# Kernel optimization log

Measured on AMD Instinct MI355X. Metric: run time of the kernel, lower is better.

Reference implementation:

```python
import jax, jax.numpy as jnp
import numpy as np

D = 896      # mm_hidden_size
H = 8        # num heads
HD = D // H  # head dim = 112
M = 8        # num_memory_tokens
P = 196      # patch_size
EPS = 1e-12


def _layernorm(x, g, b):
    mu = jnp.mean(x, axis=-1, keepdims=True)
    var = jnp.mean(jnp.square(x - mu), axis=-1, keepdims=True)
    return (x - mu) * jax.lax.rsqrt(var + EPS) * g + b


def setup_inputs() -> dict:
    key = jax.random.key(0)
    ks = jax.random.split(key, 12)
    F = 32
    s = 0.02
    return {
        "image_features": jax.random.normal(ks[0], (F, P, D), jnp.float32),
        "initial_memory": jax.random.normal(ks[1], (M, P, D), jnp.float32),
        "qW": jax.random.normal(ks[2], (D, D), jnp.float32) * s,
        "qb": jnp.zeros((D,), jnp.float32),
        "kW": jax.random.normal(ks[3], (D, D), jnp.float32) * s,
        "kb": jnp.zeros((D,), jnp.float32),
        "vW": jax.random.normal(ks[4], (D, D), jnp.float32) * s,
        "vb": jnp.zeros((D,), jnp.float32),
        "oW": jax.random.normal(ks[5], (D, D), jnp.float32) * s,
        "ob": jnp.zeros((D,), jnp.float32),
        "ln1_g": jnp.ones((D,), jnp.float32),
        "ln1_b": jnp.zeros((D,), jnp.float32),
        "mW": jax.random.normal(ks[6], (D, 4 * D), jnp.float32) * s,
        "mb": jnp.zeros((4 * D,), jnp.float32),
        "pW": jax.random.normal(ks[7], (4 * D, D), jnp.float32) * s,
        "pb": jnp.zeros((D,), jnp.float32),
        "ln2_g": jnp.ones((D,), jnp.float32),
        "ln2_b": jnp.zeros((D,), jnp.float32),
    }


def reference(image_features, initial_memory, qW, qb, kW, kb, vW, vb,
              oW, ob, ln1_g, ln1_b, mW, mb, pW, pb, ln2_g, ln2_b):
    F = image_features.shape[0]
    Lq = M * P            # 1568 query tokens
    Lk = F * P            # kv tokens
    mem = initial_memory.reshape(1, Lq, D)      # [1, Lq, D]
    img = image_features.reshape(1, Lk, D)      # [1, Lk, D]

    def heads(x, L):
        return x.reshape(1, L, H, HD).transpose(0, 2, 1, 3)  # [1,H,L,hd]

    q = heads(mem @ qW + qb, Lq)
    k = heads(img @ kW + kb, Lk)
    v = heads(img @ vW + vb, Lk)

    scores = jnp.einsum('bhqd,bhkd->bhqk', q, k) / np.sqrt(HD).astype(jnp.float32)
    probs = jax.nn.softmax(scores, axis=-1)                  # [1,H,Lq,Lk]
    ctx = jnp.einsum('bhqk,bhkd->bhqd', probs, v)
    ctx = ctx.transpose(0, 2, 1, 3).reshape(1, Lq, D)

    # residual + layernorm epilogue of Attention
    attn_out = _layernorm(ctx @ oW + ob + mem, ln1_g, ln1_b)

    # MLP -> residual + layernorm
    hidden = jax.nn.relu(attn_out @ mW + mb)                 # [1, Lq, 4D]
    out = _layernorm(hidden @ pW + pb + attn_out, ln2_g, ln2_b)

    # frame attention scores: sum over heads and query tokens, avg per frame
    attn_sum = probs.sum(axis=(1, 2))[0]                     # [Lk]
    frame_scores = attn_sum.reshape(F, P).mean(axis=1)       # [F]

    final_memory = out.reshape(M, P, D)
    return final_memory, frame_scores
```

## Files before the change

kernel.cpp:

```cpp
#include <hip/hip_runtime.h>
#include <hip/hip_bf16.h>
#include <math.h>

#define TP_D   896
#define TP_H   8
#define TP_HD  112
#define TP_LQ  1568
#define TP_LK  6272
#define TP_D4  3584
#define TP_F   32
#define TP_P   196

typedef unsigned short u16;
typedef float f32x4 __attribute__((ext_vector_type(4)));
typedef __bf16 bf16x8 __attribute__((ext_vector_type(8)));

__device__ inline float bf2f(u16 u) {
    return __uint_as_float(((unsigned int)u) << 16);
}
__device__ inline u16 f2bf(float f) {
    unsigned int x = __float_as_uint(f);
    unsigned int lsb = (x >> 16) & 1u;
    x += 0x7fffu + lsb;
    return (u16)(x >> 16);
}
__device__ inline ushort4 pack4(float a, float b, float c, float d) {
    return make_ushort4(f2bf(a), f2bf(b), f2bf(c), f2bf(d));
}
__device__ inline int pidx(int row, int col) {
    return row * 128 + (col ^ ((row & 7) << 3));
}
__device__ inline void gl_lds16(const u16* g, u16* l) {
    __builtin_amdgcn_global_load_lds(
        (const __attribute__((address_space(1))) unsigned int*)g,
        (__attribute__((address_space(3))) unsigned int*)l,
        16, 0, 0);
}

__global__ void cast2_f32_bf16(const float* __restrict__ src0, u16* __restrict__ dst0, int n0,
                               const float* __restrict__ src1, u16* __restrict__ dst1, int n1) {
    int i = (blockIdx.x * blockDim.x + threadIdx.x) * 4;
    const float* s; u16* d; int n;
    if (i < n0) { s = src0; d = dst0; n = n0; }
    else        { i -= n0; s = src1; d = dst1; n = n1; if (i >= n) return; }
    float4 v = *(const float4*)(s + i);
    *(ushort4*)(d + i) = pack4(v.x, v.y, v.z, v.w);
}

__global__ void cast_div_bf16(const float* __restrict__ src, const float* __restrict__ l,
                              u16* __restrict__ dst) {
    int i = (blockIdx.x * 256 + threadIdx.x) * 4;
    if (i >= TP_LQ * TP_D) return;
    int q = i / TP_D;
    int col = i - q * TP_D;
    int h = col / TP_HD;
    float inv = 1.f / l[h * TP_LQ + q];
    float4 v = *(const float4*)(src + i);
    *(ushort4*)(dst + i) = pack4(v.x * inv, v.y * inv, v.z * inv, v.w * inv);
}

__global__ void transpose_cast(const float* __restrict__ src, u16* __restrict__ dst, int R, int C) {
    __shared__ float t[32][33];
    int bx = blockIdx.x * 32;
    int by = blockIdx.y * 32;
    int tx = threadIdx.x, ty = threadIdx.y;
#pragma unroll
    for (int j = 0; j < 4; ++j)
        t[ty + j * 8][tx] = src[(size_t)(by + ty + j * 8) * C + bx + tx];
    __syncthreads();
#pragma unroll
    for (int j = 0; j < 4; ++j)
        dst[(size_t)(bx + ty + j * 8) * R + by + tx] = f2bf(t[tx][ty + j * 8]);
}

__global__ void transpose_cast4(const float* __restrict__ s0, u16* __restrict__ d0,
                                const float* __restrict__ s1, u16* __restrict__ d1,
                                const float* __restrict__ s2, u16* __restrict__ d2,
                                const float* __restrict__ s3, u16* __restrict__ d3) {
    __shared__ float t[32][33];
    const float* src; u16* dst;
    switch (blockIdx.z) {
        case 0: src = s0; dst = d0; break;
        case 1: src = s1; dst = d1; break;
        case 2: src = s2; dst = d2; break;
        default: src = s3; dst = d3; break;
    }
    int bx = blockIdx.x * 32;
    int by = blockIdx.y * 32;
    int tx = threadIdx.x, ty = threadIdx.y;
#pragma unroll
    for (int j = 0; j < 4; ++j)
        t[ty + j * 8][tx] = src[(size_t)(by + ty + j * 8) * TP_D + bx + tx];
    __syncthreads();
#pragma unroll
    for (int j = 0; j < 4; ++j)
        dst[(size_t)(bx + ty + j * 8) * TP_D + by + tx] = f2bf(t[tx][ty + j * 8]);
}

struct GemmParams {
    const u16* A;  int lda;
    const u16* Bt; int ldb;
    int M, N, K;
    const float* bias;
    float* outF;
    u16* outB; int ldc;
    int relu;
    int kc;
};

template <int MODE>
__global__ __launch_bounds__(256, 4) void gemm_bf16(GemmParams p) {
    __shared__ u16 lsA[128 * 32];
    __shared__ u16 lsB[64 * 32];

    const int tid = threadIdx.x;
    const int z = blockIdx.z;
    const u16* A  = p.A;
    const u16* Bt = p.Bt;
    if (MODE == 6) {
        A  += (size_t)z * p.kc;
        Bt += (size_t)z * p.kc;
    }
    const int m0 = blockIdx.y * 128;
    const int n0 = blockIdx.x * 64;

    const int lane = tid & 63;
    const int w = tid >> 6;
    const int wm = (w >> 1) * 64, wn = (w & 1) * 32;
    const int c = lane & 15, q = lane >> 4;
    const int xq = (q ^ (c & 3)) << 3;

    f32x4 acc[4][2];
#pragma unroll
    for (int i = 0; i < 4; ++i) { acc[i][0] = 0.f; acc[i][1] = 0.f; }

    const int lrow = lane >> 2;
    const int lchunk = (lane & 3) ^ (lrow & 3);
    int ga_row0 = m0 + w * 32 + lrow;      if (ga_row0 >= p.M) ga_row0 = p.M - 1;
    int ga_row1 = m0 + w * 32 + 16 + lrow; if (ga_row1 >= p.M) ga_row1 = p.M - 1;
    int gb_row  = n0 + w * 16 + lrow;      if (gb_row  >= p.N) gb_row  = p.N - 1;
    const u16* gA0 = A  + (size_t)ga_row0 * p.lda + lchunk * 8;
    const u16* gA1 = A  + (size_t)ga_row1 * p.lda + lchunk * 8;
    const u16* gB  = Bt + (size_t)gb_row  * p.ldb + lchunk * 8;
    u16* lA0 = &lsA[(w * 32) * 32];
    u16* lA1 = &lsA[(w * 32 + 16) * 32];
    u16* lB  = &lsB[(w * 16) * 32];

    const int KT = p.K >> 5;
    for (int kt = 0; kt < KT; ++kt) {
        const int k0 = kt << 5;
        gl_lds16(gA0 + k0, lA0);
        gl_lds16(gA1 + k0, lA1);
        gl_lds16(gB + k0, lB);
        __syncthreads();

        bf16x8 af[4], bfv[2];
#pragma unroll
        for (int mi = 0; mi < 4; ++mi) {
            const int r = wm + mi * 16 + c;
            af[mi] = *(const bf16x8*)(&lsA[r * 32 + xq]);
        }
#pragma unroll
        for (int ni = 0; ni < 2; ++ni) {
            const int rb = wn + ni * 16 + c;
            bfv[ni] = *(const bf16x8*)(&lsB[rb * 32 + xq]);
        }
#pragma unroll
        for (int mi = 0; mi < 4; ++mi)
#pragma unroll
            for (int ni = 0; ni < 2; ++ni)
                acc[mi][ni] = __builtin_amdgcn_mfma_f32_16x16x32_bf16(af[mi], bfv[ni], acc[mi][ni], 0, 0, 0);
        __syncthreads();
    }

#pragma unroll
    for (int mi = 0; mi < 4; ++mi) {
#pragma unroll
        for (int r = 0; r < 4; ++r) {
            const int row = m0 + wm + mi * 16 + q * 4 + r;
            if (row >= p.M) continue;
#pragma unroll
            for (int ni = 0; ni < 2; ++ni) {
                const int col = n0 + wn + ni * 16 + c;
                float v = acc[mi][ni][r];
                if (MODE == 4) {
                    v += p.bias[col];
                    if (p.relu) v = v > 0.f ? v : 0.f;
                    p.outB[(size_t)row * p.ldc + col] = f2bf(v);
                } else if (MODE == 6) {
                    atomicAdd(&p.outF[(size_t)row * p.ldc + col], v);
                }
            }
        }
    }
}

__global__ __launch_bounds__(256, 4) void qkv_proj(
        const u16* __restrict__ imgB, const u16* __restrict__ memB,
        const u16* __restrict__ kWt, const u16* __restrict__ vWt, const u16* __restrict__ qWt,
        const float* __restrict__ kb, const float* __restrict__ vb, const float* __restrict__ qb,
        u16* __restrict__ Kf, u16* __restrict__ Vtf, u16* __restrict__ Qf) {
    __shared__ u16 lsA[128 * 32];
    __shared__ u16 lsB[64 * 32];

    const int z = blockIdx.z;
    const u16* A; const u16* Bt; const float* bias; int M;
    if (z == 0)      { A = imgB; Bt = kWt; bias = kb; M = TP_LK; }
    else if (z == 1) { A = imgB; Bt = vWt; bias = vb; M = TP_LK; }
    else             { A = memB; Bt = qWt; bias = qb; M = TP_LQ; }

    const int m0 = blockIdx.y * 128;
    if (m0 >= M) return;
    const int n0 = blockIdx.x * 64;

    const int tid = threadIdx.x;
    const int lane = tid & 63;
    const int w = tid >> 6;
    const int wm = (w >> 1) * 64, wn = (w & 1) * 32;
    const int c = lane & 15, q = lane >> 4;
    const int xq = (q ^ (c & 3)) << 3;

    f32x4 acc[4][2];
#pragma unroll
    for (int i = 0; i < 4; ++i) { acc[i][0] = 0.f; acc[i][1] = 0.f; }

    const int lrow = lane >> 2;
    const int lchunk = (lane & 3) ^ (lrow & 3);
    int ga_row0 = m0 + w * 32 + lrow;      if (ga_row0 >= M) ga_row0 = M - 1;
    int ga_row1 = m0 + w * 32 + 16 + lrow; if (ga_row1 >= M) ga_row1 = M - 1;
    const int gb_row = n0 + w * 16 + lrow;
    const u16* gA0 = A  + (size_t)ga_row0 * TP_D + lchunk * 8;
    const u16* gA1 = A  + (size_t)ga_row1 * TP_D + lchunk * 8;
    const u16* gB  = Bt + (size_t)gb_row  * TP_D + lchunk * 8;
    u16* lA0 = &lsA[(w * 32) * 32];
    u16* lA1 = &lsA[(w * 32 + 16) * 32];
    u16* lB  = &lsB[(w * 16) * 32];

    for (int kt = 0; kt < 28; ++kt) {
        const int k0 = kt << 5;
        gl_lds16(gA0 + k0, lA0);
        gl_lds16(gA1 + k0, lA1);
        gl_lds16(gB + k0, lB);
        __syncthreads();

        bf16x8 af[4], bfv[2];
#pragma unroll
        for (int mi = 0; mi < 4; ++mi) {
            const int r = wm + mi * 16 + c;
            af[mi] = *(const bf16x8*)(&lsA[r * 32 + xq]);
        }
#pragma unroll
        for (int ni = 0; ni < 2; ++ni) {
            const int rb = wn + ni * 16 + c;
            bfv[ni] = *(const bf16x8*)(&lsB[rb * 32 + xq]);
        }
#pragma unroll
        for (int mi = 0; mi < 4; ++mi)
#pragma unroll
            for (int ni = 0; ni < 2; ++ni)
                acc[mi][ni] = __builtin_amdgcn_mfma_f32_16x16x32_bf16(af[mi], bfv[ni], acc[mi][ni], 0, 0, 0);
        __syncthreads();
    }

    if (z == 1) {
#pragma unroll
        for (int ni = 0; ni < 2; ++ni) {
            const int col = n0 + wn + ni * 16 + c;
            const float bv = bias[col];
#pragma unroll
            for (int mi = 0; mi < 4; ++mi) {
                const int mbase = m0 + wm + mi * 16 + q * 4;
                f32x4 a = acc[mi][ni];
                *(ushort4*)(Vtf + (size_t)col * TP_LK + mbase) =
                    pack4(a[0] + bv, a[1] + bv, a[2] + bv, a[3] + bv);
            }
        }
        return;
    }

    u16* outB = (z == 0) ? Kf : Qf;
#pragma unroll
    for (int mi = 0; mi < 4; ++mi) {
#pragma unroll
        for (int r = 0; r < 4; ++r) {
            const int row = m0 + wm + mi * 16 + q * 4 + r;
            if (row >= M) continue;
#pragma unroll
            for (int ni = 0; ni < 2; ++ni) {
                const int col = n0 + wn + ni * 16 + c;
                outB[(size_t)row * TP_D + col] = f2bf(acc[mi][ni][r] + bias[col]);
            }
        }
    }
}

__global__ __launch_bounds__(256, 2) void attn_fused(
        const u16* __restrict__ Qf, const u16* __restrict__ Kf,
        const u16* __restrict__ Vtf, u16* __restrict__ E,
        float* __restrict__ lsum, float* __restrict__ ctxF, float scale) {
    __shared__ u16 lsQ[128 * 128];
    __shared__ u16 lsB[128 * 40];
    __shared__ u16 lsP[128 * 128];

    const int ks  = blockIdx.x;
    const int m0  = blockIdx.y * 128;
    const int h   = blockIdx.z;
    const int tid = threadIdx.x;
    const int lane = tid & 63, w = tid >> 6;
    const int wm = (w >> 1) * 64, wn = (w & 1) * 64;
    const int c = lane & 15, q = lane >> 4;

    {
        const int row = tid >> 1;
        const int half = (tid & 1) * 64;
        int qrow = m0 + row; if (qrow > TP_LQ - 1) qrow = TP_LQ - 1;
        const u16* src = Qf + (size_t)qrow * TP_D + h * TP_HD;
#pragma unroll
        for (int j = 0; j < 8; ++j) {
            int col = half + j * 8;
            uint4 v = make_uint4(0, 0, 0, 0);
            if (col + 8 <= TP_HD) v = *(const uint4*)(src + col);
            *(uint4*)(&lsQ[pidx(row, col)]) = v;
        }
    }

    const int r0 = tid >> 2;
    const int c8 = (tid & 3) * 8;
    const int keybase = ks * 896;

    f32x4 acc_pv[4][4];
#pragma unroll
    for (int i = 0; i < 4; ++i)
#pragma unroll
        for (int j = 0; j < 4; ++j) acc_pv[i][j] = 0.f;
    float rs[4] = {0.f, 0.f, 0.f, 0.f};

    for (int kb = 0; kb < 7; ++kb) {
        const int kblk = keybase + kb * 128;
        f32x4 acc_s[4][4];
#pragma unroll
        for (int i = 0; i < 4; ++i)
#pragma unroll
            for (int j = 0; j < 4; ++j) acc_s[i][j] = 0.f;

#pragma unroll
        for (int kt = 0; kt < 4; ++kt) {
            const int k0 = kt * 32;
            const bool valid = (k0 + c8 + 8) <= TP_HD;
            uint4 zv = make_uint4(0, 0, 0, 0);
            uint4 vb0 = valid ? *(const uint4*)(Kf + (size_t)(kblk + r0) * TP_D + h * TP_HD + k0 + c8) : zv;
            uint4 vb1 = valid ? *(const uint4*)(Kf + (size_t)(kblk + r0 + 64) * TP_D + h * TP_HD + k0 + c8) : zv;
            __syncthreads();
            *(uint4*)(&lsB[r0 * 40 + c8])        = vb0;
            *(uint4*)(&lsB[(r0 + 64) * 40 + c8]) = vb1;
            __syncthreads();
            bf16x8 af[4], bfv[4];
#pragma unroll
            for (int mi = 0; mi < 4; ++mi)
                af[mi] = *(const bf16x8*)(&lsQ[pidx(wm + mi * 16 + c, k0 + q * 8)]);
#pragma unroll
            for (int ni = 0; ni < 4; ++ni)
                bfv[ni] = *(const bf16x8*)(&lsB[(wn + ni * 16 + c) * 40 + q * 8]);
#pragma unroll
            for (int mi = 0; mi < 4; ++mi)
#pragma unroll
                for (int ni = 0; ni < 4; ++ni)
                    acc_s[mi][ni] = __builtin_amdgcn_mfma_f32_16x16x32_bf16(bfv[ni], af[mi], acc_s[mi][ni], 0, 0, 0);
        }

        __syncthreads();
#pragma unroll
        for (int mi = 0; mi < 4; ++mi) {
            const int prow = wm + mi * 16 + c;
            const int qr = m0 + prow;
            const bool qv = qr < TP_LQ;
            float rp = 0.f;
#pragma unroll
            for (int ni = 0; ni < 4; ++ni) {
                float e0, e1, e2, e3;
                {
                    f32x4 a = acc_s[mi][ni];
                    e0 = __expf(fminf(a[0] * scale, 30.f));
                    e1 = __expf(fminf(a[1] * scale, 30.f));
                    e2 = __expf(fminf(a[2] * scale, 30.f));
                    e3 = __expf(fminf(a[3] * scale, 30.f));
                }
                rp += (e0 + e1) + (e2 + e3);
                ushort4 pk = pack4(e0, e1, e2, e3);
                const int kcol = wn + ni * 16 + q * 4;
                if (qv)
                    *(ushort4*)(E + ((size_t)h * TP_LQ + qr) * TP_LK + kblk + kcol) = pk;
                *(ushort4*)(&lsP[pidx(prow, kcol)]) = pk;
            }
            rs[mi] += rp;
        }

#pragma unroll
        for (int kt = 0; kt < 4; ++kt) {
            const int kk = kblk + kt * 32 + c8;
            int d0 = r0;
            int d1 = r0 + 64; if (d1 > TP_HD - 1) d1 = TP_HD - 1;
            uint4 vb0 = *(const uint4*)(Vtf + ((size_t)h * TP_HD + d0) * TP_LK + kk);
            uint4 vb1 = *(const uint4*)(Vtf + ((size_t)h * TP_HD + d1) * TP_LK + kk);
            __syncthreads();
            *(uint4*)(&lsB[r0 * 40 + c8])        = vb0;
            *(uint4*)(&lsB[(r0 + 64) * 40 + c8]) = vb1;
            __syncthreads();
            bf16x8 ap[4], bv[4];
#pragma unroll
            for (int mi = 0; mi < 4; ++mi)
                ap[mi] = *(const bf16x8*)(&lsP[pidx(wm + mi * 16 + c, kt * 32 + q * 8)]);
#pragma unroll
            for (int ni = 0; ni < 4; ++ni)
                bv[ni] = *(const bf16x8*)(&lsB[(wn + ni * 16 + c) * 40 + q * 8]);
#pragma unroll
            for (int mi = 0; mi < 4; ++mi)
#pragma unroll
                for (int ni = 0; ni < 4; ++ni)
                    acc_pv[mi][ni] = __builtin_amdgcn_mfma_f32_16x16x32_bf16(ap[mi], bv[ni], acc_pv[mi][ni], 0, 0, 0);
        }
    }

#pragma unroll
    for (int mi = 0; mi < 4; ++mi) {
        float rp = rs[mi];
        rp += __shfl_xor(rp, 16, 64);
        rp += __shfl_xor(rp, 32, 64);
        const int qr = m0 + wm + mi * 16 + c;
        if (q == 0 && qr < TP_LQ) atomicAdd(&lsum[h * TP_LQ + qr], rp);
    }
#pragma unroll
    for (int mi = 0; mi < 4; ++mi) {
#pragma unroll
        for (int r = 0; r < 4; ++r) {
            const int qr = m0 + wm + mi * 16 + q * 4 + r;
            if (qr >= TP_LQ) continue;
#pragma unroll
            for (int ni = 0; ni < 4; ++ni) {
                const int d = wn + ni * 16 + c;
                if (d < TP_HD)
                    atomicAdd(&ctxF[(size_t)qr * TP_D + h * TP_HD + d], acc_pv[mi][ni][r]);
            }
        }
    }
}

__global__ void colsum_kernel(const u16* __restrict__ E, const float* __restrict__ l,
                              float* __restrict__ colsum, int nrows) {
    int c4 = blockIdx.x * 256 + threadIdx.x;
    if (c4 >= TP_LK / 4) return;
    int chunk = (nrows + gridDim.y - 1) / gridDim.y;
    int r0 = blockIdx.y * chunk;
    int r1 = r0 + chunk; if (r1 > nrows) r1 = nrows;
    float a0 = 0.f, a1 = 0.f, a2 = 0.f, a3 = 0.f;
    for (int r = r0; r < r1; ++r) {
        float inv = 1.f / l[r];
        ushort4 u = ((const ushort4*)(E + (size_t)r * TP_LK))[c4];
        a0 += bf2f(u.x) * inv; a1 += bf2f(u.y) * inv;
        a2 += bf2f(u.z) * inv; a3 += bf2f(u.w) * inv;
    }
    atomicAdd(&colsum[4 * c4 + 0], a0);
    atomicAdd(&colsum[4 * c4 + 1], a1);
    atomicAdd(&colsum[4 * c4 + 2], a2);
    atomicAdd(&colsum[4 * c4 + 3], a3);
}

__global__ __launch_bounds__(256) void layernorm_rows(const float* __restrict__ x,
        const float* __restrict__ bias, const float* __restrict__ res,
        const float* __restrict__ g, const float* __restrict__ b,
        float* __restrict__ outF, u16* __restrict__ outB) {
    const int tid = threadIdx.x;
    const float* xr = x + (size_t)blockIdx.x * TP_D;
    const float* rr = res + (size_t)blockIdx.x * TP_D;
    float v[4];
#pragma unroll
    for (int i = 0; i < 4; ++i) {
        int idx = tid + i * 256;
        v[i] = (idx < TP_D) ? (xr[idx] + bias[idx] + rr[idx]) : 0.f;
    }
    float s = v[0] + v[1] + v[2] + v[3];
    __shared__ float red[4];
#pragma unroll
    for (int o = 32; o > 0; o >>= 1) s += __shfl_xor(s, o, 64);
    if ((tid & 63) == 0) red[tid >> 6] = s;
    __syncthreads();
    const float mu = (red[0] + red[1] + red[2] + red[3]) * (1.f / TP_D);
    __syncthreads();
    float ss = 0.f;
#pragma unroll
    for (int i = 0; i < 4; ++i) {
        int idx = tid + i * 256;
        if (idx < TP_D) { float d = v[i] - mu; ss += d * d; }
    }
#pragma unroll
    for (int o = 32; o > 0; o >>= 1) ss += __shfl_xor(ss, o, 64);
    if ((tid & 63) == 0) red[tid >> 6] = ss;
    __syncthreads();
    const float var = (red[0] + red[1] + red[2] + red[3]) * (1.f / TP_D);
    const float rsq = rsqrtf(var + 1e-12f);
    float* of = outF + (size_t)blockIdx.x * TP_D;
    u16* obp = outB ? outB + (size_t)blockIdx.x * TP_D : nullptr;
#pragma unroll
    for (int i = 0; i < 4; ++i) {
        int idx = tid + i * 256;
        if (idx < TP_D) {
            float y = (v[i] - mu) * rsq * g[idx] + b[idx];
            of[idx] = y;
            if (obp) obp[idx] = f2bf(y);
        }
    }
}

__global__ void frame_scores_kernel(const float* __restrict__ colsum, float* __restrict__ out) {
    const int tid = threadIdx.x;
    float v = (tid < TP_P) ? colsum[blockIdx.x * TP_P + tid] : 0.f;
    __shared__ float red[4];
#pragma unroll
    for (int o = 32; o > 0; o >>= 1) v += __shfl_xor(v, o, 64);
    if ((tid & 63) == 0) red[tid >> 6] = v;
    __syncthreads();
    if (tid == 0) out[blockIdx.x] = (red[0] + red[1] + red[2] + red[3]) * (1.f / TP_P);
}

extern "C" void kernel_launch(void* const* d_in, const int* in_sizes, int n_in,
                              void* d_out, int out_size, void* d_ws, size_t ws_size,
                              hipStream_t stream) {
    const float* img  = (const float*)d_in[0];
    const float* mem  = (const float*)d_in[1];
    const float* qW   = (const float*)d_in[2];
    const float* qb   = (const float*)d_in[3];
    const float* kW   = (const float*)d_in[4];
    const float* kb   = (const float*)d_in[5];
    const float* vW   = (const float*)d_in[6];
    const float* vb   = (const float*)d_in[7];
    const float* oW   = (const float*)d_in[8];
    const float* ob   = (const float*)d_in[9];
    const float* ln1g = (const float*)d_in[10];
    const float* ln1b = (const float*)d_in[11];
    const float* mW   = (const float*)d_in[12];
    const float* mb   = (const float*)d_in[13];
    const float* pW   = (const float*)d_in[14];
    const float* pb   = (const float*)d_in[15];
    const float* ln2g = (const float*)d_in[16];
    const float* ln2b = (const float*)d_in[17];
    float* out = (float*)d_out;

    char* base = (char*)d_ws;
    size_t off = 0;
    auto take = [&](size_t nbytes) -> void* {
        void* p = base + off;
        off += (nbytes + 255) & ~(size_t)255;
        return p;
    };

    u16* imgB  = (u16*)take((size_t)TP_LK * TP_D * 2);
    u16* memB  = (u16*)take((size_t)TP_LQ * TP_D * 2);
    u16* qWt   = (u16*)take((size_t)TP_D * TP_D * 2);
    u16* kWt   = (u16*)take((size_t)TP_D * TP_D * 2);
    u16* vWt   = (u16*)take((size_t)TP_D * TP_D * 2);
    u16* oWt   = (u16*)take((size_t)TP_D * TP_D * 2);
    u16* mWt   = (u16*)take((size_t)TP_D * TP_D4 * 2);
    u16* pWt   = (u16*)take((size_t)TP_D * TP_D4 * 2);
    u16* Qf    = (u16*)take((size_t)TP_LQ * TP_D * 2);
    u16* Kf    = (u16*)take((size_t)TP_LK * TP_D * 2);
    u16* Vtf   = (u16*)take((size_t)TP_LK * TP_D * 2);
    u16* ctxB  = (u16*)take((size_t)TP_LQ * TP_D * 2);
    float* attn  = (float*)take((size_t)TP_LQ * TP_D * 4);
    u16* attnB = (u16*)take((size_t)TP_LQ * TP_D * 2);
    u16* hidden= (u16*)take((size_t)TP_LQ * TP_D4 * 2);
    u16* E     = (u16*)take((size_t)TP_H * TP_LQ * TP_LK * 2);
    float* ctxF  = (float*)take((size_t)TP_LQ * TP_D * 4);
    float* pre1  = (float*)take((size_t)TP_LQ * TP_D * 4);
    float* pre2  = (float*)take((size_t)TP_LQ * TP_D * 4);
    float* colsum= (float*)take((size_t)TP_LK * 4);
    float* lsum  = (float*)take((size_t)TP_H * TP_LQ * 4);
    size_t zlen = (char*)(lsum + TP_H * TP_LQ) - (char*)ctxF;

    {
        int n0 = TP_LK * TP_D, n1 = TP_LQ * TP_D;
        cast2_f32_bf16<<<((n0 + n1) / 4 + 255) / 256, 256, 0, stream>>>(img, imgB, n0, mem, memB, n1);
    }
    transpose_cast4<<<dim3(28, 28, 4), dim3(32, 8), 0, stream>>>(qW, qWt, kW, kWt, vW, vWt, oW, oWt);
    transpose_cast<<<dim3(TP_D4 / 32, TP_D / 32), dim3(32, 8), 0, stream>>>(mW, mWt, TP_D, TP_D4);
    transpose_cast<<<dim3(TP_D / 32, TP_D4 / 32), dim3(32, 8), 0, stream>>>(pW, pWt, TP_D4, TP_D);
    hipMemsetAsync(ctxF, 0, zlen, stream);

    qkv_proj<<<dim3(14, 49, 3), 256, 0, stream>>>(imgB, memB, kWt, vWt, qWt,
                                                  kb, vb, qb, Kf, Vtf, Qf);

    const float scale = 0.09449111825230679f;
    attn_fused<<<dim3(7, 13, TP_H), 256, 0, stream>>>(Qf, Kf, Vtf, E, lsum, ctxF, scale);
    colsum_kernel<<<dim3(7, 448), 256, 0, stream>>>(E, lsum, colsum, TP_H * TP_LQ);
    cast_div_bf16<<<(TP_LQ * TP_D / 4 + 255) / 256, 256, 0, stream>>>(ctxF, lsum, ctxB);

    {
        GemmParams p{};
        p.A = ctxB; p.lda = TP_D;
        p.Bt = oWt; p.ldb = TP_D;
        p.M = TP_LQ; p.N = TP_D; p.K = 448; p.kc = 448;
        p.outF = pre1; p.ldc = TP_D;
        gemm_bf16<6><<<dim3(14, 13, 2), 256, 0, stream>>>(p);
    }
    layernorm_rows<<<TP_LQ, 256, 0, stream>>>(pre1, ob, mem, ln1g, ln1b, attn, attnB);

    {
        GemmParams p{};
        p.A = attnB; p.lda = TP_D;
        p.Bt = mWt; p.ldb = TP_D;
        p.M = TP_LQ; p.N = TP_D4; p.K = TP_D;
        p.bias = mb; p.outB = hidden; p.ldc = TP_D4; p.relu = 1;
        gemm_bf16<4><<<dim3(56, 13, 1), 256, 0, stream>>>(p);
    }
    {
        GemmParams p{};
        p.A = hidden; p.lda = TP_D4;
        p.Bt = pWt; p.ldb = TP_D4;
        p.M = TP_LQ; p.N = TP_D; p.K = 896; p.kc = 896;
        p.outF = pre2; p.ldc = TP_D;
        gemm_bf16<6><<<dim3(14, 13, 4), 256, 0, stream>>>(p);
    }
    layernorm_rows<<<TP_LQ, 256, 0, stream>>>(pre2, pb, attn, ln2g, ln2b, out, nullptr);

    frame_scores_kernel<<<TP_F, 256, 0, stream>>>(colsum, out + (size_t)TP_LQ * TP_D);
}
```

Baseline: 498.5 us.

## Replace materialized exp matrix with per-row per-frame partial sums

The attention kernel no longer writes the full bf16 exponent matrix (8x1568x6272) to global memory. Instead it accumulates, for each query row and head, partial sums split into the one or two frames that each 128-key block spans, and writes them into a small [H*Lq, 32] buffer with atomics. A new finalize kernel derives the row sums from these partials, normalises them and reduces to frame scores. This removes the large global write and the column-sum re-read, at the cost of extra select and shuffle work plus more atomics inside the attention kernel.

```diff
diff --git a/kernel.cpp b/kernel.cpp
--- a/kernel.cpp
+++ b/kernel.cpp
@@ -296,8 +296,8 @@
 
 __global__ __launch_bounds__(256, 2) void attn_fused(
         const u16* __restrict__ Qf, const u16* __restrict__ Kf,
-        const u16* __restrict__ Vtf, u16* __restrict__ E,
-        float* __restrict__ lsum, float* __restrict__ ctxF, float scale) {
+        const u16* __restrict__ Vtf, float* __restrict__ FQ,
+        float* __restrict__ ctxF, float scale) {
     __shared__ u16 lsQ[128 * 128];
     __shared__ u16 lsB[128 * 40];
     __shared__ u16 lsP[128 * 128];
@@ -333,7 +333,6 @@
     for (int i = 0; i < 4; ++i)
 #pragma unroll
         for (int j = 0; j < 4; ++j) acc_pv[i][j] = 0.f;
-    float rs[4] = {0.f, 0.f, 0.f, 0.f};
 
     for (int kb = 0; kb < 7; ++kb) {
         const int kblk = keybase + kb * 128;
@@ -369,30 +368,35 @@
         }
 
         __syncthreads();
+        const int fA = kblk / TP_P;
+        const int bpos = (fA + 1) * TP_P - kblk;
+        const int kq = wn + q * 4;
 #pragma unroll
         for (int mi = 0; mi < 4; ++mi) {
             const int prow = wm + mi * 16 + c;
+            float accA = 0.f, accB = 0.f;
+#pragma unroll
+            for (int ni = 0; ni < 4; ++ni) {
+                f32x4 a = acc_s[mi][ni];
+                float e0 = __expf(fminf(a[0] * scale, 30.f));
+                float e1 = __expf(fminf(a[1] * scale, 30.f));
+                float e2 = __expf(fminf(a[2] * scale, 30.f));
+                float e3 = __expf(fminf(a[3] * scale, 30.f));
+                const int kl = kq + ni * 16;
+                accA += (kl + 0 < bpos) ? e0 : 0.f;  accB += (kl + 0 < bpos) ? 0.f : e0;
+                accA += (kl + 1 < bpos) ? e1 : 0.f;  accB += (kl + 1 < bpos) ? 0.f : e1;
+                accA += (kl + 2 < bpos) ? e2 : 0.f;  accB += (kl + 2 < bpos) ? 0.f : e2;
+                accA += (kl + 3 < bpos) ? e3 : 0.f;  accB += (kl + 3 < bpos) ? 0.f : e3;
+                *(ushort4*)(&lsP[pidx(prow, kl)]) = pack4(e0, e1, e2, e3);
+            }
+            accA += __shfl_xor(accA, 16, 64); accA += __shfl_xor(accA, 32, 64);
+            accB += __shfl_xor(accB, 16, 64); accB += __shfl_xor(accB, 32, 64);
             const int qr = m0 + prow;
-            const bool qv = qr < TP_LQ;
-            float rp = 0.f;
-#pragma unroll
-            for (int ni = 0; ni < 4; ++ni) {
-                float e0, e1, e2, e3;
-                {
-                    f32x4 a = acc_s[mi][ni];
-                    e0 = __expf(fminf(a[0] * scale, 30.f));
-                    e1 = __expf(fminf(a[1] * scale, 30.f));
-                    e2 = __expf(fminf(a[2] * scale, 30.f));
-                    e3 = __expf(fminf(a[3] * scale, 30.f));
-                }
-                rp += (e0 + e1) + (e2 + e3);
-                ushort4 pk = pack4(e0, e1, e2, e3);
-                const int kcol = wn + ni * 16 + q * 4;
-                if (qv)
-                    *(ushort4*)(E + ((size_t)h * TP_LQ + qr) * TP_LK + kblk + kcol) = pk;
-                *(ushort4*)(&lsP[pidx(prow, kcol)]) = pk;
+            if (q == 0 && qr < TP_LQ) {
+                float* fq = &FQ[((size_t)h * TP_LQ + qr) * TP_F];
+                atomicAdd(fq + fA, accA);
+                if (bpos < 128) atomicAdd(fq + fA + 1, accB);
             }
-            rs[mi] += rp;
         }
 
 #pragma unroll
@@ -423,14 +427,6 @@
 
 #pragma unroll
     for (int mi = 0; mi < 4; ++mi) {
-        float rp = rs[mi];
-        rp += __shfl_xor(rp, 16, 64);
-        rp += __shfl_xor(rp, 32, 64);
-        const int qr = m0 + wm + mi * 16 + c;
-        if (q == 0 && qr < TP_LQ) atomicAdd(&lsum[h * TP_LQ + qr], rp);
-    }
-#pragma unroll
-    for (int mi = 0; mi < 4; ++mi) {
 #pragma unroll
         for (int r = 0; r < 4; ++r) {
             const int qr = m0 + wm + mi * 16 + q * 4 + r;
@@ -445,24 +441,32 @@
     }
 }
 
-__global__ void colsum_kernel(const u16* __restrict__ E, const float* __restrict__ l,
-                              float* __restrict__ colsum, int nrows) {
-    int c4 = blockIdx.x * 256 + threadIdx.x;
-    if (c4 >= TP_LK / 4) return;
-    int chunk = (nrows + gridDim.y - 1) / gridDim.y;
-    int r0 = blockIdx.y * chunk;
-    int r1 = r0 + chunk; if (r1 > nrows) r1 = nrows;
-    float a0 = 0.f, a1 = 0.f, a2 = 0.f, a3 = 0.f;
-    for (int r = r0; r < r1; ++r) {
-        float inv = 1.f / l[r];
-        ushort4 u = ((const ushort4*)(E + (size_t)r * TP_LK))[c4];
-        a0 += bf2f(u.x) * inv; a1 += bf2f(u.y) * inv;
-        a2 += bf2f(u.z) * inv; a3 += bf2f(u.w) * inv;
-    }
-    atomicAdd(&colsum[4 * c4 + 0], a0);
-    atomicAdd(&colsum[4 * c4 + 1], a1);
-    atomicAdd(&colsum[4 * c4 + 2], a2);
-    atomicAdd(&colsum[4 * c4 + 3], a3);
+__global__ __launch_bounds__(256) void frame_finalize(
+        const float* __restrict__ FQ, float* __restrict__ lsum,
+        float* __restrict__ frame_out) {
+    __shared__ float red[256 * 33];
+    const int tid = threadIdx.x;
+    const int row = blockIdx.x * 256 + tid;
+    float v[32];
+    const float4* src = (const float4*)(FQ + (size_t)row * TP_F);
+    float l = 0.f;
+#pragma unroll
+    for (int i = 0; i < 8; ++i) {
+        float4 t = src[i];
+        v[4 * i + 0] = t.x; v[4 * i + 1] = t.y;
+        v[4 * i + 2] = t.z; v[4 * i + 3] = t.w;
+        l += (t.x + t.y) + (t.z + t.w);
+    }
+    lsum[row] = l;
+    const float inv = 1.f / l;
+#pragma unroll
+    for (int f = 0; f < 32; ++f) red[tid * 33 + f] = v[f] * inv;
+    __syncthreads();
+    if (tid < 32) {
+        float s = 0.f;
+        for (int t = 0; t < 256; ++t) s += red[t * 33 + tid];
+        atomicAdd(&frame_out[tid], s * (1.f / TP_P));
+    }
 }
 
 __global__ __launch_bounds__(256) void layernorm_rows(const float* __restrict__ x,
@@ -509,17 +513,6 @@
             if (obp) obp[idx] = f2bf(y);
         }
     }
-}
-
-__global__ void frame_scores_kernel(const float* __restrict__ colsum, float* __restrict__ out) {
-    const int tid = threadIdx.x;
-    float v = (tid < TP_P) ? colsum[blockIdx.x * TP_P + tid] : 0.f;
-    __shared__ float red[4];
-#pragma unroll
-    for (int o = 32; o > 0; o >>= 1) v += __shfl_xor(v, o, 64);
-    if ((tid & 63) == 0) red[tid >> 6] = v;
-    __syncthreads();
-    if (tid == 0) out[blockIdx.x] = (red[0] + red[1] + red[2] + red[3]) * (1.f / TP_P);
 }
 
 extern "C" void kernel_launch(void* const* d_in, const int* in_sizes, int n_in,
@@ -568,13 +561,12 @@
     float* attn  = (float*)take((size_t)TP_LQ * TP_D * 4);
     u16* attnB = (u16*)take((size_t)TP_LQ * TP_D * 2);
     u16* hidden= (u16*)take((size_t)TP_LQ * TP_D4 * 2);
-    u16* E     = (u16*)take((size_t)TP_H * TP_LQ * TP_LK * 2);
+    float* lsum  = (float*)take((size_t)TP_H * TP_LQ * 4);
     float* ctxF  = (float*)take((size_t)TP_LQ * TP_D * 4);
     float* pre1  = (float*)take((size_t)TP_LQ * TP_D * 4);
     float* pre2  = (float*)take((size_t)TP_LQ * TP_D * 4);
-    float* colsum= (float*)take((size_t)TP_LK * 4);
-    float* lsum  = (float*)take((size_t)TP_H * TP_LQ * 4);
-    size_t zlen = (char*)(lsum + TP_H * TP_LQ) - (char*)ctxF;
+    float* FQ    = (float*)take((size_t)TP_H * TP_LQ * TP_F * 4);
+    size_t zlen = (char*)(FQ + (size_t)TP_H * TP_LQ * TP_F) - (char*)ctxF;
 
     {
         int n0 = TP_LK * TP_D, n1 = TP_LQ * TP_D;
@@ -584,13 +576,14 @@
     transpose_cast<<<dim3(TP_D4 / 32, TP_D / 32), dim3(32, 8), 0, stream>>>(mW, mWt, TP_D, TP_D4);
     transpose_cast<<<dim3(TP_D / 32, TP_D4 / 32), dim3(32, 8), 0, stream>>>(pW, pWt, TP_D4, TP_D);
     hipMemsetAsync(ctxF, 0, zlen, stream);
+    hipMemsetAsync(out + (size_t)TP_LQ * TP_D, 0, TP_F * 4, stream);
 
     qkv_proj<<<dim3(14, 49, 3), 256, 0, stream>>>(imgB, memB, kWt, vWt, qWt,
                                                   kb, vb, qb, Kf, Vtf, Qf);
 
     const float scale = 0.09449111825230679f;
-    attn_fused<<<dim3(7, 13, TP_H), 256, 0, stream>>>(Qf, Kf, Vtf, E, lsum, ctxF, scale);
-    colsum_kernel<<<dim3(7, 448), 256, 0, stream>>>(E, lsum, colsum, TP_H * TP_LQ);
+    attn_fused<<<dim3(7, 13, TP_H), 256, 0, stream>>>(Qf, Kf, Vtf, FQ, ctxF, scale);
+    frame_finalize<<<49, 256, 0, stream>>>(FQ, lsum, out + (size_t)TP_LQ * TP_D);
     cast_div_bf16<<<(TP_LQ * TP_D / 4 + 255) / 256, 256, 0, stream>>>(ctxF, lsum, ctxB);
 
     {
@@ -620,6 +613,4 @@
         gemm_bf16<6><<<dim3(14, 13, 4), 256, 0, stream>>>(p);
     }
     layernorm_rows<<<TP_LQ, 256, 0, stream>>>(pre2, pb, attn, ln2g, ln2b, out, nullptr);
-
-    frame_scores_kernel<<<TP_F, 256, 0, stream>>>(colsum, out + (size_t)TP_LQ * TP_D);
-}
+}
```

New measurement: 461.8 us. -7.4%, faster.
